# Performance work log

Hardware: AMD Instinct MI355X
Metric: run time of the kernel (lower is better)

The kernel has to match this reference:

```python
import jax, jax.numpy as jnp
import numpy as np

B, T, C = 4, 2048, 2048
H, N = 32, 64          # n_head, head_size; H*N == C (n_dim_att == n_dim)
DMIX, DDEC = 32, 64    # hardcoded LoRA dims in module


def setup_inputs() -> dict:
    key = jax.random.key(0)
    ks = jax.random.split(key, 24)
    u = lambda k, s, lo, hi: jax.random.uniform(k, s, jnp.float32, lo, hi)
    g = lambda k, s: jax.random.normal(k, s, jnp.float32) * 0.02
    return {
        'x': jax.random.normal(ks[0], (B, T, C), jnp.float32),
        'shift_state_in': jax.random.normal(ks[1], (B, C), jnp.float32),
        'wkv_state_in': jnp.zeros((B, H, N, N), jnp.float32),
        'time_maa_x': u(ks[2], (C,), 0.0, 1.0),
        'time_maa_r': u(ks[3], (C,), 0.0, 1.0),
        'time_maa_k': u(ks[4], (C,), 0.0, 1.0),
        'time_maa_v': u(ks[5], (C,), 0.0, 1.0),
        'time_maa_w': u(ks[6], (C,), 0.0, 1.0),
        'time_maa_v2': u(ks[7], (C,), 0.0, 1.0),
        'time_maa_w1': u(ks[8], (C, DMIX * 5), -0.01, 0.01),
        'time_maa_w2': u(ks[9], (5, DMIX, C), -0.01, 0.01),
        'time_decay': u(ks[10], (C,), -6.0, -1.0),
        'time_decay_w1': u(ks[11], (C, DDEC), -0.01, 0.01),
        'time_decay_w2': u(ks[12], (DDEC, C), -0.01, 0.01),
        'time_value2_w1': u(ks[13], (C, DDEC), -0.01, 0.01),
        'time_value2_w2': u(ks[14], (DDEC, C), -0.01, 0.01),
        'W_r': g(ks[15], (C, C)),
        'W_k': g(ks[16], (C, C)),
        'W_v': g(ks[17], (C, C)),
        'W_o': g(ks[18], (C, C)),
        'ln_w': jnp.ones((C,), jnp.float32),
        'ln_b': jnp.zeros((C,), jnp.float32),
    }


def _to_heads(a):
    # [B,T,C] -> [T,B,H,N] for time-major scan
    return a.reshape(B, T, H, N).transpose(1, 0, 2, 3)


def reference(x, shift_state_in, wkv_state_in,
              time_maa_x, time_maa_r, time_maa_k, time_maa_v, time_maa_w, time_maa_v2,
              time_maa_w1, time_maa_w2,
              time_decay, time_decay_w1, time_decay_w2,
              time_value2_w1, time_value2_w2,
              W_r, W_k, W_v, W_o, ln_w, ln_b):
    # token shift
    dxprev = jnp.concatenate([shift_state_in[:, None, :], x[:, :-1]], axis=1) - x
    xxx = x + dxprev * time_maa_x
    hmix = jnp.tanh(xxx @ time_maa_w1).reshape(B, T, 5, DMIX)
    mix = jnp.einsum('btfd,fdc->fbtc', hmix, time_maa_w2)  # [5,B,T,C]
    mr, mk, mv, mw, mv2 = mix
    xr = x + dxprev * (time_maa_r + mr)
    xk = x + dxprev * (time_maa_k + mk)
    xv = x + dxprev * (time_maa_v + mv)
    xw = x + dxprev * (time_maa_w + mw)
    xv2 = x + dxprev * (time_maa_v2 + mv2)

    r = xr @ W_r
    k = xk @ W_k
    v = xv @ W_v
    v2 = xv2 @ W_v + jnp.tanh(xv2 @ time_value2_w1) @ time_value2_w2
    w = time_decay + jnp.tanh(xw @ time_decay_w1) @ time_decay_w2
    decay = jnp.exp(-jnp.exp(w))         # per-channel, data-dependent
    k = k * (1.0 - decay)

    rh, kh, vh, dh = _to_heads(r), _to_heads(k), _to_heads(v), _to_heads(decay)

    def step(state, inputs):
        # state: [B,H,N,N] (k-dim x v-dim); u (time_faaaa) is zero in this variant
        r_t, k_t, v_t, d_t = inputs  # each [B,H,N]
        y = jnp.einsum('bhi,bhij->bhj', r_t, state)
        state = state * d_t[..., None] + k_t[..., None] * v_t[..., None, :]
        return state, y

    wkv_state_out, ys = jax.lax.scan(step, wkv_state_in, (rh, kh, vh, dh))
    y = ys.transpose(1, 0, 2, 3).reshape(B, T, C)
    y = y + v2
    # LayerNorm over n_dim_att
    mu = jnp.mean(y, axis=-1, keepdims=True)
    var = jnp.var(y, axis=-1, keepdims=True)
    y = (y - mu) / jnp.sqrt(var + 1e-5) * ln_w + ln_b
    y = y @ W_o
    return y, x[:, -1], wkv_state_out
```

## Files before the change

### kernel.cpp

```cpp
#include <hip/hip_runtime.h>
#include <hip/hip_bf16.h>
#include <cstdio>


typedef __attribute__((ext_vector_type(8))) short bf16x8;
typedef __attribute__((ext_vector_type(4))) float floatx4;

#define T_DIM 2048
#define C_DIM 2048
#define B_DIM 4
#define M_ROWS (B_DIM * T_DIM)

typedef const unsigned int __attribute__((address_space(1)))* gas1_t;
typedef unsigned int __attribute__((address_space(3)))* las3_t;
__device__ __forceinline__ void gl_lds16(const void* g, void* l) {
    __builtin_amdgcn_global_load_lds((gas1_t)g, (las3_t)l, 16, 0, 0);
}

__global__ __launch_bounds__(256) void k_transpose(
    const float* __restrict__ in, void* __restrict__ out,
    int R, int Cin, int to_bf16)
{
    __shared__ float tile[32][33];
    const int tx = threadIdx.x & 31, ty = threadIdx.x >> 5;
    const int cbase = blockIdx.x * 32, rbase = blockIdx.y * 32;
#pragma unroll
    for (int i = 0; i < 4; i++) {
        int r = rbase + ty + i * 8;
        int c = cbase + tx;
        tile[ty + i * 8][tx] = (c < Cin) ? in[(size_t)r * Cin + c] : 0.0f;
    }
    __syncthreads();
    if (to_bf16) {
        __hip_bfloat16* ob = (__hip_bfloat16*)out;
#pragma unroll
        for (int i = 0; i < 4; i++) {
            int c = cbase + ty + i * 8;
            ob[(size_t)c * R + rbase + tx] = __float2bfloat16(tile[tx][ty + i * 8]);
        }
    } else {
        float* of = (float*)out;
#pragma unroll
        for (int i = 0; i < 4; i++) {
            int c = cbase + ty + i * 8;
            of[(size_t)c * R + rbase + tx] = tile[tx][ty + i * 8];
        }
    }
}

__global__ __launch_bounds__(256) void k_xx(
    const float* __restrict__ x, const float* __restrict__ shift,
    const float* __restrict__ tmx,
    __hip_bfloat16* __restrict__ XX, float* __restrict__ xlast)
{
    const int row = blockIdx.x;
    const int b = row >> 11, t = row & 2047;
    const int c0 = threadIdx.x * 8;
    const float* xrow = x + (size_t)row * C_DIM;
    const float* prow = (t == 0) ? (shift + (size_t)b * C_DIM) : (xrow - C_DIM);
    float4 xa = ((const float4*)(xrow + c0))[0];
    float4 xb = ((const float4*)(xrow + c0))[1];
    float4 pa = ((const float4*)(prow + c0))[0];
    float4 pb = ((const float4*)(prow + c0))[1];
    float xv8[8] = {xa.x, xa.y, xa.z, xa.w, xb.x, xb.y, xb.z, xb.w};
    float pv8[8] = {pa.x, pa.y, pa.z, pa.w, pb.x, pb.y, pb.z, pb.w};
    union { bf16x8 v8; __hip_bfloat16 e[8]; } u;
#pragma unroll
    for (int j = 0; j < 8; j++)
        u.e[j] = __float2bfloat16(fmaf(pv8[j] - xv8[j], tmx[c0 + j], xv8[j]));
    *(bf16x8*)(XX + (size_t)row * C_DIM + c0) = u.v8;
    if (t == T_DIM - 1) {
        ((float4*)(xlast + (size_t)b * C_DIM + c0))[0] = xa;
        ((float4*)(xlast + (size_t)b * C_DIM + c0))[1] = xb;
    }
}

__global__ __launch_bounds__(256) void k_gemm_h(
    const __hip_bfloat16* __restrict__ A,
    const __hip_bfloat16* __restrict__ Bt,
    float* __restrict__ Hout)
{
    __shared__ __hip_bfloat16 As[64 * 32];
    __shared__ __hip_bfloat16 Bs[256 * 32];
    const int tid = threadIdx.x;
    const int m0 = blockIdx.x * 64;
    const int wave = tid >> 6, lane = tid & 63;
    const int fcol = lane & 15, quad = lane >> 4;
    floatx4 acc[16];
#pragma unroll
    for (int i = 0; i < 16; i++) acc[i] = (floatx4){0.f, 0.f, 0.f, 0.f};

    const int rA = tid >> 2, kcA = (tid & 3) * 8;
    const __hip_bfloat16* gA = A + (size_t)(m0 + rA) * 2048 + kcA;
    __hip_bfloat16* lA = As + tid * 8;
    const __hip_bfloat16* gB[4];
    __hip_bfloat16* lB[4];
#pragma unroll
    for (int s = 0; s < 4; s++) {
        int q = tid + 256 * s;
        gB[s] = Bt + (size_t)(q >> 2) * 2048 + (q & 3) * 8;
        lB[s] = Bs + q * 8;
    }
    for (int kk = 0; kk < 2048; kk += 32) {
        gl_lds16(gA + kk, lA);
#pragma unroll
        for (int s = 0; s < 4; s++) gl_lds16(gB[s] + kk, lB[s]);
        __syncthreads();
        bf16x8 aF = *(const bf16x8*)(As + (wave * 16 + fcol) * 32 + quad * 8);
#pragma unroll
        for (int ni = 0; ni < 16; ni++) {
            bf16x8 bF = *(const bf16x8*)(Bs + (ni * 16 + fcol) * 32 + quad * 8);
            acc[ni] = __builtin_amdgcn_mfma_f32_16x16x32_bf16(aF, bF, acc[ni], 0, 0, 0);
        }
        __syncthreads();
    }
#pragma unroll
    for (int ni = 0; ni < 16; ni++) {
        int col = ni * 16 + fcol;
#pragma unroll
        for (int g = 0; g < 4; g++) {
            int row = m0 + wave * 16 + quad * 4 + g;
            Hout[(size_t)row * 256 + col] = tanhf(acc[ni][g]);
        }
    }
}

__global__ __launch_bounds__(256) void k_gemm_n64(
    const __hip_bfloat16* __restrict__ A,
    const __hip_bfloat16* __restrict__ Bt,
    __hip_bfloat16* __restrict__ G)
{
    __shared__ __hip_bfloat16 As[64 * 32];
    __shared__ __hip_bfloat16 Bs[64 * 32];
    const int tid = threadIdx.x;
    const int m0 = blockIdx.x * 64;
    const int wave = tid >> 6, lane = tid & 63;
    const int fcol = lane & 15, quad = lane >> 4;
    floatx4 acc[4];
#pragma unroll
    for (int i = 0; i < 4; i++) acc[i] = (floatx4){0.f, 0.f, 0.f, 0.f};

    const int r = tid >> 2, kc = (tid & 3) * 8;
    const __hip_bfloat16* gA = A + (size_t)(m0 + r) * 2048 + kc;
    const __hip_bfloat16* gB = Bt + (size_t)r * 2048 + kc;
    __hip_bfloat16* lA = As + tid * 8;
    __hip_bfloat16* lB = Bs + tid * 8;
    for (int kk = 0; kk < 2048; kk += 32) {
        gl_lds16(gA + kk, lA);
        gl_lds16(gB + kk, lB);
        __syncthreads();
        bf16x8 aF = *(const bf16x8*)(As + (wave * 16 + fcol) * 32 + quad * 8);
#pragma unroll
        for (int ni = 0; ni < 4; ni++) {
            bf16x8 bF = *(const bf16x8*)(Bs + (ni * 16 + fcol) * 32 + quad * 8);
            acc[ni] = __builtin_amdgcn_mfma_f32_16x16x32_bf16(aF, bF, acc[ni], 0, 0, 0);
        }
        __syncthreads();
    }
#pragma unroll
    for (int ni = 0; ni < 4; ni++) {
        int col = ni * 16 + fcol;
#pragma unroll
        for (int g = 0; g < 4; g++) {
            int row = m0 + wave * 16 + quad * 4 + g;
            G[(size_t)row * 64 + col] = __float2bfloat16(tanhf(acc[ni][g]));
        }
    }
}

__global__ __launch_bounds__(256) void k_mixapply(
    const float* __restrict__ x, const float* __restrict__ shift,
    const float* __restrict__ H, const float* __restrict__ w2,
    const float* __restrict__ tmr, const float* __restrict__ tmk,
    const float* __restrict__ tmv, const float* __restrict__ tmw,
    const float* __restrict__ tmv2,
    __hip_bfloat16* __restrict__ xr, __hip_bfloat16* __restrict__ xk,
    __hip_bfloat16* __restrict__ xv, __hip_bfloat16* __restrict__ xw,
    __hip_bfloat16* __restrict__ xv2)
{
    __shared__ float hsm[16][160];
    const int row0 = blockIdx.x * 16;
    const int b = row0 >> 11;
    const int tid = threadIdx.x;
    for (int idx = tid; idx < 16 * 160; idx += 256)
        hsm[idx / 160][idx % 160] = H[(size_t)(row0 + idx / 160) * 256 + idx % 160];
    __syncthreads();
    const int c0 = tid * 8;
    const float* maas[5] = {tmr, tmk, tmv, tmw, tmv2};
    __hip_bfloat16* outs[5] = {xr, xk, xv, xw, xv2};
    for (int rc = 0; rc < 16; rc += 8) {
#pragma unroll
        for (int f = 0; f < 5; f++) {
            float acc[8][8];
#pragma unroll
            for (int r = 0; r < 8; r++)
#pragma unroll
                for (int j = 0; j < 8; j++) acc[r][j] = 0.f;
#pragma unroll 4
            for (int d = 0; d < 32; d++) {
                const float4* wp = (const float4*)(w2 + (size_t)(f * 32 + d) * 2048 + c0);
                float4 p0 = wp[0], p1 = wp[1];
                float wv[8] = {p0.x, p0.y, p0.z, p0.w, p1.x, p1.y, p1.z, p1.w};
#pragma unroll
                for (int r = 0; r < 8; r++) {
                    float h = hsm[rc + r][f * 32 + d];
#pragma unroll
                    for (int j = 0; j < 8; j++) acc[r][j] = fmaf(h, wv[j], acc[r][j]);
                }
            }
            const float* maa = maas[f];
            float m8[8];
#pragma unroll
            for (int j = 0; j < 8; j++) m8[j] = maa[c0 + j];
#pragma unroll
            for (int r = 0; r < 8; r++) {
                int row = row0 + rc + r;
                int t = row & 2047;
                const float* xrow = x + (size_t)row * C_DIM;
                const float* prow = (t == 0) ? (shift + (size_t)b * C_DIM) : (xrow - C_DIM);
                float4 xa = ((const float4*)(xrow + c0))[0];
                float4 xb = ((const float4*)(xrow + c0))[1];
                float4 pa = ((const float4*)(prow + c0))[0];
                float4 pb = ((const float4*)(prow + c0))[1];
                float xv8[8] = {xa.x, xa.y, xa.z, xa.w, xb.x, xb.y, xb.z, xb.w};
                float pv8[8] = {pa.x, pa.y, pa.z, pa.w, pb.x, pb.y, pb.z, pb.w};
                union { bf16x8 v8; __hip_bfloat16 e[8]; } u;
#pragma unroll
                for (int j = 0; j < 8; j++) {
                    float dx = pv8[j] - xv8[j];
                    u.e[j] = __float2bfloat16(fmaf(dx, m8[j] + acc[r][j], xv8[j]));
                }
                *(bf16x8*)(outs[f] + (size_t)row * C_DIM + c0) = u.v8;
            }
        }
    }
}

__global__ __launch_bounds__(256) void k_gemm(
    const __hip_bfloat16* __restrict__ A,
    const __hip_bfloat16* __restrict__ Bt,
    int mode,
    float* __restrict__ outF, __hip_bfloat16* __restrict__ outB)
{
    constexpr int K = 2048;
    __shared__ __hip_bfloat16 As[128 * 32];
    __shared__ __hip_bfloat16 Bs[128 * 32];
    const int tid = threadIdx.x;
    const int id = blockIdx.x;
    const int xcd = id & 7, jj = id >> 3;
    const int m0 = (((xcd << 3) | (jj & 7))) * 128;
    const int n0 = (jj >> 3) * 128;
    const int wave = tid >> 6, lane = tid & 63;
    const int wm = (wave >> 1) * 64, wn = (wave & 1) * 64;
    const int fcol = lane & 15, quad = lane >> 4;

    floatx4 acc[4][4];
#pragma unroll
    for (int mi = 0; mi < 4; mi++)
#pragma unroll
        for (int ni = 0; ni < 4; ni++)
            acc[mi][ni] = (floatx4){0.f, 0.f, 0.f, 0.f};

    const int q0 = tid, q1 = tid + 256;
    const int r0 = q0 >> 2, kc0 = (q0 & 3) * 8;
    const int r1 = q1 >> 2, kc1 = (q1 & 3) * 8;
    const __hip_bfloat16* gA0 = A + (size_t)(m0 + r0) * K + kc0;
    const __hip_bfloat16* gA1 = A + (size_t)(m0 + r1) * K + kc1;
    const __hip_bfloat16* gB0 = Bt + (size_t)(n0 + r0) * K + kc0;
    const __hip_bfloat16* gB1 = Bt + (size_t)(n0 + r1) * K + kc1;
    __hip_bfloat16* lA0 = As + q0 * 8; __hip_bfloat16* lA1 = As + q1 * 8;
    __hip_bfloat16* lB0 = Bs + q0 * 8; __hip_bfloat16* lB1 = Bs + q1 * 8;

    for (int kk = 0; kk < K; kk += 32) {
        gl_lds16(gA0 + kk, lA0);
        gl_lds16(gA1 + kk, lA1);
        gl_lds16(gB0 + kk, lB0);
        gl_lds16(gB1 + kk, lB1);
        __syncthreads();
        bf16x8 aF[4], bF[4];
#pragma unroll
        for (int mi = 0; mi < 4; mi++)
            aF[mi] = *(const bf16x8*)(As + (wm + mi * 16 + fcol) * 32 + quad * 8);
#pragma unroll
        for (int ni = 0; ni < 4; ni++)
            bF[ni] = *(const bf16x8*)(Bs + (wn + ni * 16 + fcol) * 32 + quad * 8);
#pragma unroll
        for (int mi = 0; mi < 4; mi++)
#pragma unroll
            for (int ni = 0; ni < 4; ni++)
                acc[mi][ni] = __builtin_amdgcn_mfma_f32_16x16x32_bf16(
                    aF[mi], bF[ni], acc[mi][ni], 0, 0, 0);
        __syncthreads();
    }
#pragma unroll
    for (int mi = 0; mi < 4; mi++) {
#pragma unroll
        for (int ni = 0; ni < 4; ni++) {
            int rbase = m0 + wm + mi * 16 + quad * 4;
            int ccol = n0 + wn + ni * 16 + fcol;
#pragma unroll
            for (int g = 0; g < 4; g++) {
                size_t idx = (size_t)(rbase + g) * 2048 + ccol;
                float val = acc[mi][ni][g];
                if (mode == 0) outF[idx] = val;
                else           outB[idx] = __float2bfloat16(val);
            }
        }
    }
}

__global__ __launch_bounds__(256) void k_gemm64(
    const __hip_bfloat16* __restrict__ A0, const __hip_bfloat16* __restrict__ B0,
    const __hip_bfloat16* __restrict__ A1, const __hip_bfloat16* __restrict__ B1,
    float* __restrict__ decayOut, const float* __restrict__ tdec,
    __hip_bfloat16* __restrict__ v2Out)
{
    constexpr int K = 64;
    __shared__ __hip_bfloat16 As[128 * 32];
    __shared__ __hip_bfloat16 Bs[128 * 32];
    const int tid = threadIdx.x;
    const int op = blockIdx.x >> 10;
    const int id = blockIdx.x & 1023;
    const int xcd = id & 7, jj = id >> 3;
    const int m0 = (((xcd << 3) | (jj & 7))) * 128;
    const int n0 = (jj >> 3) * 128;
    const __hip_bfloat16* A = op ? A1 : A0;
    const __hip_bfloat16* Bt = op ? B1 : B0;
    const int wave = tid >> 6, lane = tid & 63;
    const int wm = (wave >> 1) * 64, wn = (wave & 1) * 64;
    const int fcol = lane & 15, quad = lane >> 4;

    floatx4 acc[4][4];
#pragma unroll
    for (int mi = 0; mi < 4; mi++)
#pragma unroll
        for (int ni = 0; ni < 4; ni++)
            acc[mi][ni] = (floatx4){0.f, 0.f, 0.f, 0.f};

    const int q0 = tid, q1 = tid + 256;
    const int r0 = q0 >> 2, kc0 = (q0 & 3) * 8;
    const int r1 = q1 >> 2, kc1 = (q1 & 3) * 8;
    const __hip_bfloat16* gA0 = A + (size_t)(m0 + r0) * K + kc0;
    const __hip_bfloat16* gA1 = A + (size_t)(m0 + r1) * K + kc1;
    const __hip_bfloat16* gB0 = Bt + (size_t)(n0 + r0) * K + kc0;
    const __hip_bfloat16* gB1 = Bt + (size_t)(n0 + r1) * K + kc1;
    __hip_bfloat16* lA0 = As + q0 * 8; __hip_bfloat16* lA1 = As + q1 * 8;
    __hip_bfloat16* lB0 = Bs + q0 * 8; __hip_bfloat16* lB1 = Bs + q1 * 8;

    for (int kk = 0; kk < K; kk += 32) {
        gl_lds16(gA0 + kk, lA0);
        gl_lds16(gA1 + kk, lA1);
        gl_lds16(gB0 + kk, lB0);
        gl_lds16(gB1 + kk, lB1);
        __syncthreads();
        bf16x8 aF[4], bF[4];
#pragma unroll
        for (int mi = 0; mi < 4; mi++)
            aF[mi] = *(const bf16x8*)(As + (wm + mi * 16 + fcol) * 32 + quad * 8);
#pragma unroll
        for (int ni = 0; ni < 4; ni++)
            bF[ni] = *(const bf16x8*)(Bs + (wn + ni * 16 + fcol) * 32 + quad * 8);
#pragma unroll
        for (int mi = 0; mi < 4; mi++)
#pragma unroll
            for (int ni = 0; ni < 4; ni++)
                acc[mi][ni] = __builtin_amdgcn_mfma_f32_16x16x32_bf16(
                    aF[mi], bF[ni], acc[mi][ni], 0, 0, 0);
        __syncthreads();
    }
#pragma unroll
    for (int mi = 0; mi < 4; mi++) {
#pragma unroll
        for (int ni = 0; ni < 4; ni++) {
            int rbase = m0 + wm + mi * 16 + quad * 4;
            int ccol = n0 + wn + ni * 16 + fcol;
#pragma unroll
            for (int g = 0; g < 4; g++) {
                size_t idx = (size_t)(rbase + g) * 2048 + ccol;
                float val = acc[mi][ni][g];
                if (op == 0) {
                    decayOut[idx] = expf(-expf(val + tdec[ccol]));
                } else {
                    v2Out[idx] = __float2bfloat16(__bfloat162float(v2Out[idx]) + val);
                }
            }
        }
    }
}

__global__ __launch_bounds__(256) void k_scan_chunked(
    const __hip_bfloat16* __restrict__ r, const __hip_bfloat16* __restrict__ k,
    const __hip_bfloat16* __restrict__ v, const float* __restrict__ dec,
    const float* __restrict__ state_in,
    __hip_bfloat16* __restrict__ y, float* __restrict__ state_out)
{
    __shared__ __hip_bfloat16 Rs[64 * 64];
    __shared__ __hip_bfloat16 Ks[64 * 64];
    __shared__ __hip_bfloat16 Vs[64 * 64];
    __shared__ float Ds[64 * 64];
    __shared__ __hip_bfloat16 Am[64 * 72];
    __shared__ __hip_bfloat16 Bm[64 * 72];
    __shared__ __hip_bfloat16 VT[64 * 72];
    __shared__ __hip_bfloat16 CT[64 * 72];
    __shared__ __hip_bfloat16 ST[64 * 72];
    __shared__ __hip_bfloat16 Pm[64 * 72];
    __shared__ float part[4][64];
    __shared__ float efin[64];

    const int tid = threadIdx.x;
    const int bh = blockIdx.x, b = bh >> 5, h = bh & 31;
    const int wave = tid >> 6, lane = tid & 63;
    const int fcol = lane & 15, quad = lane >> 4;
    const int ci = tid & 63, seg = tid >> 6;

    floatx4 sfr[4];
    {
        const float* sp = state_in + (size_t)bh * 4096;
#pragma unroll
        for (int n = 0; n < 4; n++)
#pragma unroll
            for (int g = 0; g < 4; g++)
                sfr[n][g] = sp[(size_t)(16 * wave + quad * 4 + g) * 64 + 16 * n + fcol];
    }

    const size_t cbase0 = (size_t)b * T_DIM * C_DIM + (size_t)h * 64;
    for (int c = 0; c < 32; c++) {
        const size_t cb = cbase0 + (size_t)c * 64 * C_DIM;
        {
            const int q0 = tid, q1 = tid + 256;
            gl_lds16(r + cb + (size_t)(q0 >> 3) * C_DIM + (q0 & 7) * 8, Rs + q0 * 8);
            gl_lds16(r + cb + (size_t)(q1 >> 3) * C_DIM + (q1 & 7) * 8, Rs + q1 * 8);
            gl_lds16(k + cb + (size_t)(q0 >> 3) * C_DIM + (q0 & 7) * 8, Ks + q0 * 8);
            gl_lds16(k + cb + (size_t)(q1 >> 3) * C_DIM + (q1 & 7) * 8, Ks + q1 * 8);
            gl_lds16(v + cb + (size_t)(q0 >> 3) * C_DIM + (q0 & 7) * 8, Vs + q0 * 8);
            gl_lds16(v + cb + (size_t)(q1 >> 3) * C_DIM + (q1 & 7) * 8, Vs + q1 * 8);
#pragma unroll
            for (int s = 0; s < 4; s++) {
                int q = tid + 256 * s;
                gl_lds16(dec + cb + (size_t)(q >> 4) * C_DIM + (q & 15) * 4, Ds + q * 4);
            }
        }
        __syncthreads();

        {
#pragma unroll
            for (int n = 0; n < 4; n++)
#pragma unroll
                for (int g = 0; g < 4; g++)
                    ST[(size_t)(16 * n + fcol) * 72 + 16 * wave + quad * 4 + g] =
                        __float2bfloat16(sfr[n][g]);
            float p = 1.0f;
#pragma unroll
            for (int u = 0; u < 16; u++) p *= Ds[(seg * 16 + u) * 64 + ci];
            part[seg][ci] = p;
        }
        __syncthreads();

        {
            float p0 = part[0][ci], p1 = part[1][ci], p2 = part[2][ci], p3 = part[3][ci];
            float pre = 1.0f;
            if (seg > 0) pre *= p0;
            if (seg > 1) pre *= p1;
            if (seg > 2) pre *= p2;
            float tot = p0 * p1 * p2 * p3;
            if (seg == 0) efin[ci] = tot;
            float e = pre;
#pragma unroll
            for (int u = 0; u < 16; u++) {
                int t = seg * 16 + u;
                float d = Ds[t * 64 + ci];
                float rv = __bfloat162float(Rs[t * 64 + ci]);
                float kv = __bfloat162float(Ks[t * 64 + ci]) * (1.0f - d);
                Am[t * 72 + ci] = __float2bfloat16(rv * e);
                e *= d;
                float bb = kv * __builtin_amdgcn_rcpf(e);
                Bm[t * 72 + ci] = __float2bfloat16(bb);
                CT[ci * 72 + t] = __float2bfloat16(bb * tot);
            }
#pragma unroll
            for (int u = 0; u < 16; u++) {
                int t = seg * 16 + ((u + (ci & 15)) & 15);
                VT[ci * 72 + t] = Vs[t * 64 + ci];
            }
        }
        __syncthreads();

        {
            bf16x8 af[2];
#pragma unroll
            for (int kk = 0; kk < 2; kk++)
                af[kk] = *(const bf16x8*)(Am + (16 * wave + fcol) * 72 + kk * 32 + quad * 8);
            floatx4 pfr[4], yfr[4];
#pragma unroll
            for (int n = 0; n < 4; n++) {
                pfr[n] = (floatx4){0.f, 0.f, 0.f, 0.f};
                yfr[n] = (floatx4){0.f, 0.f, 0.f, 0.f};
#pragma unroll
                for (int kk = 0; kk < 2; kk++) {
                    bf16x8 bF = *(const bf16x8*)(Bm + (16 * n + fcol) * 72 + kk * 32 + quad * 8);
                    bf16x8 sF = *(const bf16x8*)(ST + (16 * n + fcol) * 72 + kk * 32 + quad * 8);
                    pfr[n] = __builtin_amdgcn_mfma_f32_16x16x32_bf16(af[kk], bF, pfr[n], 0, 0, 0);
                    yfr[n] = __builtin_amdgcn_mfma_f32_16x16x32_bf16(af[kk], sF, yfr[n], 0, 0, 0);
                }
            }
#pragma unroll
            for (int n = 0; n < 4; n++)
#pragma unroll
                for (int g = 0; g < 4; g++) {
                    int t = 16 * wave + quad * 4 + g;
                    int s = 16 * n + fcol;
                    Pm[t * 72 + s] = (s < t) ? __float2bfloat16(pfr[n][g])
                                             : __float2bfloat16(0.0f);
                }
            float eg[4];
#pragma unroll
            for (int g = 0; g < 4; g++) eg[g] = efin[16 * wave + quad * 4 + g];
#pragma unroll
            for (int n = 0; n < 4; n++)
#pragma unroll
                for (int g = 0; g < 4; g++) sfr[n][g] *= eg[g];
            bf16x8 pf[2], cf[2];
#pragma unroll
            for (int kk = 0; kk < 2; kk++) {
                pf[kk] = *(const bf16x8*)(Pm + (16 * wave + fcol) * 72 + kk * 32 + quad * 8);
                cf[kk] = *(const bf16x8*)(CT + (16 * wave + fcol) * 72 + kk * 32 + quad * 8);
            }
#pragma unroll
            for (int n = 0; n < 4; n++) {
#pragma unroll
                for (int kk = 0; kk < 2; kk++) {
                    bf16x8 vF = *(const bf16x8*)(VT + (16 * n + fcol) * 72 + kk * 32 + quad * 8);
                    yfr[n] = __builtin_amdgcn_mfma_f32_16x16x32_bf16(pf[kk], vF, yfr[n], 0, 0, 0);
                    sfr[n] = __builtin_amdgcn_mfma_f32_16x16x32_bf16(cf[kk], vF, sfr[n], 0, 0, 0);
                }
            }
#pragma unroll
            for (int n = 0; n < 4; n++)
#pragma unroll
                for (int g = 0; g < 4; g++) {
                    size_t addr = cb + (size_t)(16 * wave + quad * 4 + g) * C_DIM + 16 * n + fcol;
                    float yv = __bfloat162float(y[addr]) + yfr[n][g];
                    y[addr] = __float2bfloat16(yv);
                }
        }
    }
    {
        float* so = state_out + (size_t)bh * 4096;
#pragma unroll
        for (int n = 0; n < 4; n++)
#pragma unroll
            for (int g = 0; g < 4; g++)
                so[(size_t)(16 * wave + quad * 4 + g) * 64 + 16 * n + fcol] = sfr[n][g];
    }
}

__global__ __launch_bounds__(256) void k_addln(
    __hip_bfloat16* __restrict__ y,
    const float* __restrict__ lnw, const float* __restrict__ lnb)
{
    __shared__ float ls[4], ls2[4];
    const int row = blockIdx.x;
    const size_t base = (size_t)row * C_DIM;
    const int tid = threadIdx.x;
    const int c0 = tid * 8;
    union { bf16x8 v8; __hip_bfloat16 e[8]; } uin;
    uin.v8 = *(const bf16x8*)(y + base + c0);
    float vbuf[8];
#pragma unroll
    for (int j = 0; j < 8; j++) vbuf[j] = __bfloat162float(uin.e[j]);
    float s = 0.f, s2 = 0.f;
#pragma unroll
    for (int j = 0; j < 8; j++) { s += vbuf[j]; s2 += vbuf[j] * vbuf[j]; }
#pragma unroll
    for (int off = 32; off > 0; off >>= 1) {
        s += __shfl_down(s, off, 64);
        s2 += __shfl_down(s2, off, 64);
    }
    const int w = tid >> 6;
    if ((tid & 63) == 0) { ls[w] = s; ls2[w] = s2; }
    __syncthreads();
    float S = ls[0] + ls[1] + ls[2] + ls[3];
    float S2 = ls2[0] + ls2[1] + ls2[2] + ls2[3];
    float mu = S * (1.0f / C_DIM);
    float var = S2 * (1.0f / C_DIM) - mu * mu;
    float rs = rsqrtf(var + 1e-5f);
    union { bf16x8 v8; __hip_bfloat16 e[8]; } u;
#pragma unroll
    for (int j = 0; j < 8; j++) {
        int ccc = c0 + j;
        u.e[j] = __float2bfloat16((vbuf[j] - mu) * rs * lnw[ccc] + lnb[ccc]);
    }
    *(bf16x8*)(y + base + c0) = u.v8;
}

extern "C" void kernel_launch(void* const* d_in, const int* in_sizes, int n_in,
                              void* d_out, int out_size, void* d_ws, size_t ws_size,
                              hipStream_t stream)
{
    const float* x     = (const float*)d_in[0];
    const float* shift = (const float*)d_in[1];
    const float* wkvin = (const float*)d_in[2];
    const float* tmx   = (const float*)d_in[3];
    const float* tmr   = (const float*)d_in[4];
    const float* tmk   = (const float*)d_in[5];
    const float* tmv   = (const float*)d_in[6];
    const float* tmw   = (const float*)d_in[7];
    const float* tmv2  = (const float*)d_in[8];
    const float* w1    = (const float*)d_in[9];
    const float* w2    = (const float*)d_in[10];
    const float* tdec  = (const float*)d_in[11];
    const float* dw1   = (const float*)d_in[12];
    const float* dw2   = (const float*)d_in[13];
    const float* vw1   = (const float*)d_in[14];
    const float* vw2   = (const float*)d_in[15];
    const float* Wr    = (const float*)d_in[16];
    const float* Wk    = (const float*)d_in[17];
    const float* Wv    = (const float*)d_in[18];
    const float* Wo    = (const float*)d_in[19];
    const float* lnw   = (const float*)d_in[20];
    const float* lnb   = (const float*)d_in[21];

    const size_t SZ_XBF = (size_t)M_ROWS * C_DIM * 2;
    const size_t SZ_WBF = (size_t)C_DIM * C_DIM * 2;
    char* ws = (char*)d_ws;
    size_t off = 0;
    __hip_bfloat16* S0 = (__hip_bfloat16*)(ws + off); off += SZ_XBF;
    __hip_bfloat16* S1 = (__hip_bfloat16*)(ws + off); off += SZ_XBF;
    __hip_bfloat16* S2 = (__hip_bfloat16*)(ws + off); off += SZ_XBF;
    __hip_bfloat16* S3 = (__hip_bfloat16*)(ws + off); off += SZ_XBF;
    __hip_bfloat16* S4 = (__hip_bfloat16*)(ws + off); off += SZ_XBF;
    char* D = ws + off; off += (size_t)M_ROWS * C_DIM * 4;
    __hip_bfloat16* XX    = (__hip_bfloat16*)D;
    float*          Hbuf  = (float*)(D + SZ_XBF);
    float*          decay = (float*)D;
    __hip_bfloat16* WrT = (__hip_bfloat16*)(ws + off); off += SZ_WBF;
    __hip_bfloat16* WkT = (__hip_bfloat16*)(ws + off); off += SZ_WBF;
    __hip_bfloat16* WvT = (__hip_bfloat16*)(ws + off); off += SZ_WBF;
    __hip_bfloat16* WoT = (__hip_bfloat16*)(ws + off); off += SZ_WBF;
    __hip_bfloat16* w1tb  = (__hip_bfloat16*)(ws + off); off += (size_t)256 * 2048 * 2;
    __hip_bfloat16* dw1t  = (__hip_bfloat16*)(ws + off); off += (size_t)64 * 2048 * 2;
    __hip_bfloat16* vw1t  = (__hip_bfloat16*)(ws + off); off += (size_t)64 * 2048 * 2;
    __hip_bfloat16* dw2t  = (__hip_bfloat16*)(ws + off); off += (size_t)2048 * 64 * 2;
    __hip_bfloat16* vw2t  = (__hip_bfloat16*)(ws + off); off += (size_t)2048 * 64 * 2;
    __hip_bfloat16* Gd    = (__hip_bfloat16*)(ws + off); off += (size_t)M_ROWS * 64 * 2;
    __hip_bfloat16* Gv    = (__hip_bfloat16*)(ws + off); off += (size_t)M_ROWS * 64 * 2;
    if (ws_size < off) {
        fprintf(stderr, "kernel_launch: ws too small (%zu < %zu)\n", ws_size, off);
        return;
    }

    float* out_y     = (float*)d_out;
    float* out_xlast = out_y + (size_t)M_ROWS * C_DIM;
    float* out_state = out_xlast + (size_t)B_DIM * C_DIM;

    k_transpose<<<dim3(8, 64),  256, 0, stream>>>(w1,  w1tb, 2048, 160, 1);
    k_transpose<<<dim3(2, 64),  256, 0, stream>>>(dw1, dw1t, 2048, 64, 1);
    k_transpose<<<dim3(2, 64),  256, 0, stream>>>(vw1, vw1t, 2048, 64, 1);
    k_transpose<<<dim3(64, 2),  256, 0, stream>>>(dw2, dw2t, 64, 2048, 1);
    k_transpose<<<dim3(64, 2),  256, 0, stream>>>(vw2, vw2t, 64, 2048, 1);
    k_transpose<<<dim3(64, 64), 256, 0, stream>>>(Wr, WrT, 2048, 2048, 1);
    k_transpose<<<dim3(64, 64), 256, 0, stream>>>(Wk, WkT, 2048, 2048, 1);
    k_transpose<<<dim3(64, 64), 256, 0, stream>>>(Wv, WvT, 2048, 2048, 1);
    k_transpose<<<dim3(64, 64), 256, 0, stream>>>(Wo, WoT, 2048, 2048, 1);

    k_xx<<<M_ROWS, 256, 0, stream>>>(x, shift, tmx, XX, out_xlast);
    k_gemm_h<<<128, 256, 0, stream>>>(XX, w1tb, Hbuf);
    k_mixapply<<<512, 256, 0, stream>>>(x, shift, Hbuf, w2,
                                        tmr, tmk, tmv, tmw, tmv2,
                                        S0, S1, S2, S3, S4);
    k_gemm_n64<<<128, 256, 0, stream>>>(S3, dw1t, Gd);
    k_gemm_n64<<<128, 256, 0, stream>>>(S4, vw1t, Gv);
    k_gemm<<<1024, 256, 0, stream>>>(S1, WkT, 1, nullptr, S3);
    k_gemm<<<1024, 256, 0, stream>>>(S0, WrT, 1, nullptr, S1);
    k_gemm<<<1024, 256, 0, stream>>>(S2, WvT, 1, nullptr, S0);
    k_gemm<<<1024, 256, 0, stream>>>(S4, WvT, 1, nullptr, S2);
    k_gemm64<<<2048, 256, 0, stream>>>(Gd, dw2t, Gv, vw2t, decay, tdec, S2);
    k_scan_chunked<<<128, 256, 0, stream>>>(S1, S3, S0, decay, wkvin, S2, out_state);
    k_addln<<<M_ROWS, 256, 0, stream>>>(S2, lnw, lnb);
    k_gemm<<<1024, 256, 0, stream>>>(S2, WoT, 0, out_y, nullptr);

    (void)in_sizes; (void)n_in; (void)out_size;
}
```

Before: 1.295 ms.

## Use 256x256 GEMM tiles with a 4-stage async LDS pipeline

Replaces the 128x128 single-buffered bf16 GEMM with a 256x256 tile kernel using 512 threads and a 4-slot LDS ring. Global-to-LDS loads are issued three stages ahead, with explicit vmcnt waits and a single barrier per k-step. The aim is to hide memory latency behind the MFMAs and to cut global traffic per flop through larger tiles. In exchange it uses 128 KB of LDS and more accumulator registers, and launches only 256 blocks, which may leave some CUs underused.

```diff
diff --git a/kernel.cpp b/kernel.cpp
--- a/kernel.cpp
+++ b/kernel.cpp
@@ -236,64 +236,78 @@
     }
 }
 
-__global__ __launch_bounds__(256) void k_gemm(
+__global__ __launch_bounds__(512, 2) void k_gemm256(
     const __hip_bfloat16* __restrict__ A,
     const __hip_bfloat16* __restrict__ Bt,
     int mode,
     float* __restrict__ outF, __hip_bfloat16* __restrict__ outB)
 {
     constexpr int K = 2048;
-    __shared__ __hip_bfloat16 As[128 * 32];
-    __shared__ __hip_bfloat16 Bs[128 * 32];
+    constexpr int NT = K / 32;
+    __shared__ __hip_bfloat16 LA[4][256 * 32];
+    __shared__ __hip_bfloat16 LB[4][256 * 32];
     const int tid = threadIdx.x;
-    const int id = blockIdx.x;
-    const int xcd = id & 7, jj = id >> 3;
-    const int m0 = (((xcd << 3) | (jj & 7))) * 128;
-    const int n0 = (jj >> 3) * 128;
+    const int bid = blockIdx.x;
+    const int n0 = (bid & 7) * 256;
+    const int m0 = (bid >> 3) * 256;
     const int wave = tid >> 6, lane = tid & 63;
-    const int wm = (wave >> 1) * 64, wn = (wave & 1) * 64;
+    const int wm = (wave >> 2) * 128, wn = (wave & 3) * 64;
     const int fcol = lane & 15, quad = lane >> 4;
 
-    floatx4 acc[4][4];
-#pragma unroll
-    for (int mi = 0; mi < 4; mi++)
+    floatx4 acc[8][4];
+#pragma unroll
+    for (int mi = 0; mi < 8; mi++)
 #pragma unroll
         for (int ni = 0; ni < 4; ni++)
             acc[mi][ni] = (floatx4){0.f, 0.f, 0.f, 0.f};
 
-    const int q0 = tid, q1 = tid + 256;
-    const int r0 = q0 >> 2, kc0 = (q0 & 3) * 8;
-    const int r1 = q1 >> 2, kc1 = (q1 & 3) * 8;
-    const __hip_bfloat16* gA0 = A + (size_t)(m0 + r0) * K + kc0;
-    const __hip_bfloat16* gA1 = A + (size_t)(m0 + r1) * K + kc1;
-    const __hip_bfloat16* gB0 = Bt + (size_t)(n0 + r0) * K + kc0;
-    const __hip_bfloat16* gB1 = Bt + (size_t)(n0 + r1) * K + kc1;
-    __hip_bfloat16* lA0 = As + q0 * 8; __hip_bfloat16* lA1 = As + q1 * 8;
-    __hip_bfloat16* lB0 = Bs + q0 * 8; __hip_bfloat16* lB1 = Bs + q1 * 8;
-
-    for (int kk = 0; kk < K; kk += 32) {
-        gl_lds16(gA0 + kk, lA0);
-        gl_lds16(gA1 + kk, lA1);
-        gl_lds16(gB0 + kk, lB0);
-        gl_lds16(gB1 + kk, lB1);
-        __syncthreads();
-        bf16x8 aF[4], bF[4];
-#pragma unroll
-        for (int mi = 0; mi < 4; mi++)
-            aF[mi] = *(const bf16x8*)(As + (wm + mi * 16 + fcol) * 32 + quad * 8);
+    const int ch0 = wave * 2, ch1 = wave * 2 + 1;
+    const int rr = lane >> 2, kc = (lane & 3) * 8;
+    const __hip_bfloat16* pA0 = A  + (size_t)(m0 + ch0 * 16 + rr) * K + kc;
+    const __hip_bfloat16* pA1 = A  + (size_t)(m0 + ch1 * 16 + rr) * K + kc;
+    const __hip_bfloat16* pB0 = Bt + (size_t)(n0 + ch0 * 16 + rr) * K + kc;
+    const __hip_bfloat16* pB1 = Bt + (size_t)(n0 + ch1 * 16 + rr) * K + kc;
+    const int lo0 = ch0 * 512 + lane * 8;
+    const int lo1 = ch1 * 512 + lane * 8;
+
+    int ns = 0;
+    for (; ns < 3; ++ns) {
+        gl_lds16(pA0 + ns * 32, &LA[ns][lo0]);
+        gl_lds16(pA1 + ns * 32, &LA[ns][lo1]);
+        gl_lds16(pB0 + ns * 32, &LB[ns][lo0]);
+        gl_lds16(pB1 + ns * 32, &LB[ns][lo1]);
+    }
+    for (int t = 0; t < NT; ++t) {
+        if (t < NT - 2)       asm volatile("s_waitcnt vmcnt(8)" ::: "memory");
+        else if (t == NT - 2) asm volatile("s_waitcnt vmcnt(4)" ::: "memory");
+        else                  asm volatile("s_waitcnt vmcnt(0)" ::: "memory");
+        asm volatile("s_barrier" ::: "memory");
+        if (ns < NT) {
+            const int sl = ns & 3;
+            gl_lds16(pA0 + ns * 32, &LA[sl][lo0]);
+            gl_lds16(pA1 + ns * 32, &LA[sl][lo1]);
+            gl_lds16(pB0 + ns * 32, &LB[sl][lo0]);
+            gl_lds16(pB1 + ns * 32, &LB[sl][lo1]);
+            ++ns;
+        }
+        const int st = t & 3;
+        const __hip_bfloat16* ab = &LA[st][(wm + fcol) * 32 + quad * 8];
+        const __hip_bfloat16* bb = &LB[st][(wn + fcol) * 32 + quad * 8];
+        bf16x8 bF[4];
 #pragma unroll
         for (int ni = 0; ni < 4; ni++)
-            bF[ni] = *(const bf16x8*)(Bs + (wn + ni * 16 + fcol) * 32 + quad * 8);
-#pragma unroll
-        for (int mi = 0; mi < 4; mi++)
+            bF[ni] = *(const bf16x8*)(bb + ni * 512);
+#pragma unroll
+        for (int mi = 0; mi < 8; mi++) {
+            bf16x8 aF = *(const bf16x8*)(ab + mi * 512);
 #pragma unroll
             for (int ni = 0; ni < 4; ni++)
                 acc[mi][ni] = __builtin_amdgcn_mfma_f32_16x16x32_bf16(
-                    aF[mi], bF[ni], acc[mi][ni], 0, 0, 0);
-        __syncthreads();
-    }
-#pragma unroll
-    for (int mi = 0; mi < 4; mi++) {
+                    aF, bF[ni], acc[mi][ni], 0, 0, 0);
+        }
+    }
+#pragma unroll
+    for (int mi = 0; mi < 8; mi++) {
 #pragma unroll
         for (int ni = 0; ni < 4; ni++) {
             int rbase = m0 + wm + mi * 16 + quad * 4;
@@ -670,14 +684,14 @@
                                         S0, S1, S2, S3, S4);
     k_gemm_n64<<<128, 256, 0, stream>>>(S3, dw1t, Gd);
     k_gemm_n64<<<128, 256, 0, stream>>>(S4, vw1t, Gv);
-    k_gemm<<<1024, 256, 0, stream>>>(S1, WkT, 1, nullptr, S3);
-    k_gemm<<<1024, 256, 0, stream>>>(S0, WrT, 1, nullptr, S1);
-    k_gemm<<<1024, 256, 0, stream>>>(S2, WvT, 1, nullptr, S0);
-    k_gemm<<<1024, 256, 0, stream>>>(S4, WvT, 1, nullptr, S2);
+    k_gemm256<<<256, 512, 0, stream>>>(S1, WkT, 1, nullptr, S3);
+    k_gemm256<<<256, 512, 0, stream>>>(S0, WrT, 1, nullptr, S1);
+    k_gemm256<<<256, 512, 0, stream>>>(S2, WvT, 1, nullptr, S0);
+    k_gemm256<<<256, 512, 0, stream>>>(S4, WvT, 1, nullptr, S2);
     k_gemm64<<<2048, 256, 0, stream>>>(Gd, dw2t, Gv, vw2t, decay, tdec, S2);
     k_scan_chunked<<<128, 256, 0, stream>>>(S1, S3, S0, decay, wkvin, S2, out_state);
     k_addln<<<M_ROWS, 256, 0, stream>>>(S2, lnw, lnb);
-    k_gemm<<<1024, 256, 0, stream>>>(S2, WoT, 0, out_y, nullptr);
+    k_gemm256<<<256, 512, 0, stream>>>(S2, WoT, 0, out_y, nullptr);
 
     (void)in_sizes; (void)n_in; (void)out_size;
 }
```

New measurement: 1.233 ms. 1.05x faster.
